# Kernel tuning notes

Hardware: AMD Instinct MI355X
Metric: run time of the kernel (lower is better)

## Reference

```python
import jax, jax.numpy as jnp
import numpy as np


def setup_inputs() -> dict:
    key = jax.random.key(0)
    k1, k2 = jax.random.split(key)
    B, C, H, W_, P = 32, 256, 64, 64, 8
    x = jax.random.normal(k1, (B, C, H, W_), dtype=jnp.float32)
    # 1x1 conv weight [P, C] and bias [P], init like torch Conv2d default
    bound = 1.0 / np.sqrt(C)
    W = jax.random.uniform(k2, (P, C), dtype=jnp.float32, minval=-bound, maxval=bound)
    b = jnp.zeros((P,), dtype=jnp.float32)
    return {"x": x, "W": W, "b": b}


def reference(x, W, b):
    B, C, H, Wd = x.shape
    P = W.shape[0]
    # 1x1 conv: scores[b,p,h,w] = sum_c W[p,c] * x[b,c,h,w] + b[p]
    scores = jnp.einsum('pc,bchw->bphw', W, x) + b[None, :, None, None]
    # spatial softmax over HW
    part_maps = jax.nn.softmax(scores.reshape(B, P, H * Wd), axis=2).reshape(B, P, H, Wd)
    # fused per-part weighted average pool: mean over HW of x * map
    pooled = jnp.einsum('bchw,bphw->bpc', x, part_maps) / (H * Wd)  # [B,P,C]
    return pooled.reshape(B, P * C)
```

## Files before the change

kernel.cpp:

```cpp
#include <hip/hip_runtime.h>

#define HW 4096
#define NC 256
#define NP 8
#define NB 32
#define CHW 64
#define NCH 64

#define FMA4(acc, v, s)                  \
  acc.x = fmaf((v).x, (s), acc.x);       \
  acc.y = fmaf((v).y, (s), acc.y);       \
  acc.z = fmaf((v).z, (s), acc.z);       \
  acc.w = fmaf((v).w, (s), acc.w)

__global__ __launch_bounds__(256) void k_fused(
    const float* __restrict__ x, const float* __restrict__ Wm,
    const float* __restrict__ bias, float* __restrict__ partial,
    float* __restrict__ psum) {
  __shared__ __align__(16) float wt[NC][NP];
  __shared__ __align__(16) float sp[4][NP][CHW];
  __shared__ __align__(16) float els[NP][68];

  const int bid = blockIdx.x;
  const int b = bid >> 6;
  const int chunk = bid & 63;
  const int t = threadIdx.x, lane = t & 63, w = t >> 6;
  const float* xb = x + (size_t)b * NC * HW + chunk * CHW;

#pragma unroll
  for (int p = 0; p < NP; ++p) wt[t][p] = Wm[p * NC + t];
  __syncthreads();

  const int cr = lane >> 4;
  const int q = lane & 15;
  const int c0 = w << 6;
  const float* xwp = xb + (size_t)(c0 + cr) * HW + q * 4;

  float4 s4[NP];
#pragma unroll
  for (int p = 0; p < NP; ++p) s4[p] = make_float4(0.f, 0.f, 0.f, 0.f);

#pragma unroll
  for (int h = 0; h < 2; ++h) {
    float4 xv[8];
#pragma unroll
    for (int i = 0; i < 8; ++i)
      xv[i] = *(const float4*)(xwp + (size_t)(h * 32 + i * 4) * HW);
#pragma unroll
    for (int i = 0; i < 8; ++i) {
      int c = c0 + h * 32 + i * 4 + cr;
      float4 wA = *(const float4*)&wt[c][0];
      float4 wB = *(const float4*)&wt[c][4];
      FMA4(s4[0], xv[i], wA.x);
      FMA4(s4[1], xv[i], wA.y);
      FMA4(s4[2], xv[i], wA.z);
      FMA4(s4[3], xv[i], wA.w);
      FMA4(s4[4], xv[i], wB.x);
      FMA4(s4[5], xv[i], wB.y);
      FMA4(s4[6], xv[i], wB.z);
      FMA4(s4[7], xv[i], wB.w);
    }
  }

#pragma unroll
  for (int p = 0; p < NP; ++p) {
    float4 v = s4[p];
    v.x += __shfl_xor(v.x, 16); v.y += __shfl_xor(v.y, 16);
    v.z += __shfl_xor(v.z, 16); v.w += __shfl_xor(v.w, 16);
    v.x += __shfl_xor(v.x, 32); v.y += __shfl_xor(v.y, 32);
    v.z += __shfl_xor(v.z, 32); v.w += __shfl_xor(v.w, 32);
    if (cr == 0) *(float4*)&sp[w][p][q * 4] = v;
  }
  __syncthreads();

  {
    const int ep = t >> 5, eh = t & 31;
    float a0 = bias[ep], a1 = a0;
#pragma unroll
    for (int ww = 0; ww < 4; ++ww) {
      a0 += sp[ww][ep][eh];
      a1 += sp[ww][ep][eh + 32];
    }
    float e0 = expf(a0), e1 = expf(a1);
    els[ep][eh] = e0;
    els[ep][eh + 32] = e1;
    float esum = e0 + e1;
#pragma unroll
    for (int off = 16; off; off >>= 1) esum += __shfl_xor(esum, off);
    if (eh == 0) psum[bid * NP + ep] = esum;
  }
  __syncthreads();

  const float* xr = xb + (size_t)t * HW;
  float acc[NP];
#pragma unroll
  for (int p = 0; p < NP; ++p) acc[p] = 0.f;

#pragma unroll
  for (int h = 0; h < 2; ++h) {
    float4 xv[8];
#pragma unroll
    for (int j = 0; j < 8; ++j)
      xv[j] = *(const float4*)(xr + (h * 8 + j) * 4);
#pragma unroll
    for (int j = 0; j < 8; ++j) {
      const int k = h * 8 + j;
#pragma unroll
      for (int p = 0; p < NP; ++p) {
        float4 e4 = *(const float4*)&els[p][k * 4];
        acc[p] = fmaf(xv[j].x, e4.x, acc[p]);
        acc[p] = fmaf(xv[j].y, e4.y, acc[p]);
        acc[p] = fmaf(xv[j].z, e4.z, acc[p]);
        acc[p] = fmaf(xv[j].w, e4.w, acc[p]);
      }
    }
  }

#pragma unroll
  for (int p = 0; p < NP; ++p)
    partial[((size_t)bid * NP + p) * NC + t] = acc[p];
}

__global__ __launch_bounds__(256) void k_reduce(
    const float* __restrict__ partial, const float* __restrict__ psum,
    float* __restrict__ out) {
  int bp = blockIdx.x;
  int b = bp >> 3, p = bp & 7;
  int t = threadIdx.x, lane = t & 63, w2 = t >> 6;

  __shared__ float gv;
  if (w2 == 0) {
    float v = psum[(size_t)(b * NCH + lane) * NP + p];
#pragma unroll
    for (int off = 32; off; off >>= 1) v += __shfl_xor(v, off);
    if (lane == 0) gv = 1.0f / (v * (float)HW);
  }
  __syncthreads();
  float ginv = gv;

  float acc = 0.f;
#pragma unroll 16
  for (int ch = 0; ch < NCH; ++ch)
    acc += partial[(((size_t)b * NCH + ch) * NP + p) * NC + t];
  out[((size_t)b * NP + p) * NC + t] = acc * ginv;
}

extern "C" void kernel_launch(void* const* d_in, const int* in_sizes, int n_in,
                              void* d_out, int out_size, void* d_ws, size_t ws_size,
                              hipStream_t stream) {
  const float* x = (const float*)d_in[0];
  const float* Wm = (const float*)d_in[1];
  const float* bias = (const float*)d_in[2];
  float* out = (float*)d_out;

  float* ws = (float*)d_ws;
  float* partial = ws;
  float* psum = ws + (size_t)NB * NCH * NP * NC;

  k_fused<<<NB * NCH, 256, 0, stream>>>(x, Wm, bias, partial, psum);
  k_reduce<<<NB * NP, 256, 0, stream>>>(partial, psum, out);
}
```

Measured before the change: 52.31 us.

## Process two 64-pixel subchunks per block, prefetching second subchunk during pooling

Each block now covers 128 spatial positions as two 64-wide subchunks, which halves the block count and the size of the partial buffer that the reduce kernel must sum. The first half of the second subchunk's x loads is issued before the first subchunk's pooling pass, so those global reads overlap with compute. It uses double-buffered exp tiles in shared memory and accumulates pooled sums across both subchunks. In exchange, the prefetched registers raise register pressure, and there are fewer blocks to fill the GPU.

```diff
diff --git a/kernel.cpp b/kernel.cpp
--- a/kernel.cpp
+++ b/kernel.cpp
@@ -4,8 +4,9 @@
 #define NC 256
 #define NP 8
 #define NB 32
-#define CHW 64
-#define NCH 64
+#define SUB 64
+#define CHW 128
+#define NCH (HW / CHW)
 
 #define FMA4(acc, v, s)                  \
   acc.x = fmaf((v).x, (s), acc.x);       \
@@ -13,17 +14,33 @@
   acc.z = fmaf((v).z, (s), acc.z);       \
   acc.w = fmaf((v).w, (s), acc.w)
 
+#define A_BATCH(xvarr, hbase)                                  \
+  _Pragma("unroll")                                            \
+  for (int i = 0; i < 8; ++i) {                                \
+    int c = c0 + (hbase) + i * 4 + cr;                         \
+    float4 wA = *(const float4*)&wt[c][0];                     \
+    float4 wB = *(const float4*)&wt[c][4];                     \
+    FMA4(s4[0], xvarr[i], wA.x);                               \
+    FMA4(s4[1], xvarr[i], wA.y);                               \
+    FMA4(s4[2], xvarr[i], wA.z);                               \
+    FMA4(s4[3], xvarr[i], wA.w);                               \
+    FMA4(s4[4], xvarr[i], wB.x);                               \
+    FMA4(s4[5], xvarr[i], wB.y);                               \
+    FMA4(s4[6], xvarr[i], wB.z);                               \
+    FMA4(s4[7], xvarr[i], wB.w);                               \
+  }
+
 __global__ __launch_bounds__(256) void k_fused(
     const float* __restrict__ x, const float* __restrict__ Wm,
     const float* __restrict__ bias, float* __restrict__ partial,
     float* __restrict__ psum) {
   __shared__ __align__(16) float wt[NC][NP];
-  __shared__ __align__(16) float sp[4][NP][CHW];
-  __shared__ __align__(16) float els[NP][68];
+  __shared__ __align__(16) float sp[4][NP][SUB];
+  __shared__ __align__(16) float els[2][NP][68];
 
   const int bid = blockIdx.x;
-  const int b = bid >> 6;
-  const int chunk = bid & 63;
+  const int b = bid >> 5;
+  const int chunk = bid & 31;
   const int t = threadIdx.x, lane = t & 63, w = t >> 6;
   const float* xb = x + (size_t)b * NC * HW + chunk * CHW;
 
@@ -34,34 +51,28 @@
   const int cr = lane >> 4;
   const int q = lane & 15;
   const int c0 = w << 6;
-  const float* xwp = xb + (size_t)(c0 + cr) * HW + q * 4;
+  const int ep = t >> 5, eh = t & 31;
+  const float bia = bias[ep];
+  const float* xwp0 = xb + (size_t)(c0 + cr) * HW + q * 4;
+  const float* xwp1 = xwp0 + SUB;
+  const float* xr = xb + (size_t)t * HW;
+
+  float acc[NP];
+#pragma unroll
+  for (int p = 0; p < NP; ++p) acc[p] = 0.f;
+  float esum_tot = 0.f;
 
   float4 s4[NP];
 #pragma unroll
   for (int p = 0; p < NP; ++p) s4[p] = make_float4(0.f, 0.f, 0.f, 0.f);
-
 #pragma unroll
   for (int h = 0; h < 2; ++h) {
     float4 xv[8];
 #pragma unroll
     for (int i = 0; i < 8; ++i)
-      xv[i] = *(const float4*)(xwp + (size_t)(h * 32 + i * 4) * HW);
-#pragma unroll
-    for (int i = 0; i < 8; ++i) {
-      int c = c0 + h * 32 + i * 4 + cr;
-      float4 wA = *(const float4*)&wt[c][0];
-      float4 wB = *(const float4*)&wt[c][4];
-      FMA4(s4[0], xv[i], wA.x);
-      FMA4(s4[1], xv[i], wA.y);
-      FMA4(s4[2], xv[i], wA.z);
-      FMA4(s4[3], xv[i], wA.w);
-      FMA4(s4[4], xv[i], wB.x);
-      FMA4(s4[5], xv[i], wB.y);
-      FMA4(s4[6], xv[i], wB.z);
-      FMA4(s4[7], xv[i], wB.w);
-    }
-  }
-
+      xv[i] = *(const float4*)(xwp0 + (size_t)(h * 32 + i * 4) * HW);
+    A_BATCH(xv, h * 32)
+  }
 #pragma unroll
   for (int p = 0; p < NP; ++p) {
     float4 v = s4[p];
@@ -74,27 +85,23 @@
   __syncthreads();
 
   {
-    const int ep = t >> 5, eh = t & 31;
-    float a0 = bias[ep], a1 = a0;
+    float a0 = bia, a1 = bia;
 #pragma unroll
     for (int ww = 0; ww < 4; ++ww) {
       a0 += sp[ww][ep][eh];
       a1 += sp[ww][ep][eh + 32];
     }
     float e0 = expf(a0), e1 = expf(a1);
-    els[ep][eh] = e0;
-    els[ep][eh + 32] = e1;
-    float esum = e0 + e1;
-#pragma unroll
-    for (int off = 16; off; off >>= 1) esum += __shfl_xor(esum, off);
-    if (eh == 0) psum[bid * NP + ep] = esum;
-  }
-  __syncthreads();
-
-  const float* xr = xb + (size_t)t * HW;
-  float acc[NP];
-#pragma unroll
-  for (int p = 0; p < NP; ++p) acc[p] = 0.f;
+    els[0][ep][eh] = e0;
+    els[0][ep][eh + 32] = e1;
+    esum_tot += e0 + e1;
+  }
+  __syncthreads();
+
+  float4 xp[8];
+#pragma unroll
+  for (int i = 0; i < 8; ++i)
+    xp[i] = *(const float4*)(xwp1 + (size_t)(i * 4) * HW);
 
 #pragma unroll
   for (int h = 0; h < 2; ++h) {
@@ -107,7 +114,7 @@
       const int k = h * 8 + j;
 #pragma unroll
       for (int p = 0; p < NP; ++p) {
-        float4 e4 = *(const float4*)&els[p][k * 4];
+        float4 e4 = *(const float4*)&els[0][p][k * 4];
         acc[p] = fmaf(xv[j].x, e4.x, acc[p]);
         acc[p] = fmaf(xv[j].y, e4.y, acc[p]);
         acc[p] = fmaf(xv[j].z, e4.z, acc[p]);
@@ -117,8 +124,67 @@
   }
 
 #pragma unroll
+  for (int p = 0; p < NP; ++p) s4[p] = make_float4(0.f, 0.f, 0.f, 0.f);
+  A_BATCH(xp, 0)
+  {
+    float4 xv[8];
+#pragma unroll
+    for (int i = 0; i < 8; ++i)
+      xv[i] = *(const float4*)(xwp1 + (size_t)(32 + i * 4) * HW);
+    A_BATCH(xv, 32)
+  }
+#pragma unroll
+  for (int p = 0; p < NP; ++p) {
+    float4 v = s4[p];
+    v.x += __shfl_xor(v.x, 16); v.y += __shfl_xor(v.y, 16);
+    v.z += __shfl_xor(v.z, 16); v.w += __shfl_xor(v.w, 16);
+    v.x += __shfl_xor(v.x, 32); v.y += __shfl_xor(v.y, 32);
+    v.z += __shfl_xor(v.z, 32); v.w += __shfl_xor(v.w, 32);
+    if (cr == 0) *(float4*)&sp[w][p][q * 4] = v;
+  }
+  __syncthreads();
+
+  {
+    float a0 = bia, a1 = bia;
+#pragma unroll
+    for (int ww = 0; ww < 4; ++ww) {
+      a0 += sp[ww][ep][eh];
+      a1 += sp[ww][ep][eh + 32];
+    }
+    float e0 = expf(a0), e1 = expf(a1);
+    els[1][ep][eh] = e0;
+    els[1][ep][eh + 32] = e1;
+    esum_tot += e0 + e1;
+  }
+  __syncthreads();
+
+#pragma unroll
+  for (int h = 0; h < 2; ++h) {
+    float4 xv[8];
+#pragma unroll
+    for (int j = 0; j < 8; ++j)
+      xv[j] = *(const float4*)(xr + SUB + (h * 8 + j) * 4);
+#pragma unroll
+    for (int j = 0; j < 8; ++j) {
+      const int k = h * 8 + j;
+#pragma unroll
+      for (int p = 0; p < NP; ++p) {
+        float4 e4 = *(const float4*)&els[1][p][k * 4];
+        acc[p] = fmaf(xv[j].x, e4.x, acc[p]);
+        acc[p] = fmaf(xv[j].y, e4.y, acc[p]);
+        acc[p] = fmaf(xv[j].z, e4.z, acc[p]);
+        acc[p] = fmaf(xv[j].w, e4.w, acc[p]);
+      }
+    }
+  }
+
+#pragma unroll
   for (int p = 0; p < NP; ++p)
     partial[((size_t)bid * NP + p) * NC + t] = acc[p];
+
+#pragma unroll
+  for (int off = 16; off; off >>= 1) esum_tot += __shfl_xor(esum_tot, off);
+  if (eh == 0) psum[bid * NP + ep] = esum_tot;
 }
 
 __global__ __launch_bounds__(256) void k_reduce(
@@ -130,9 +196,9 @@
 
   __shared__ float gv;
   if (w2 == 0) {
-    float v = psum[(size_t)(b * NCH + lane) * NP + p];
-#pragma unroll
-    for (int off = 32; off; off >>= 1) v += __shfl_xor(v, off);
+    float v = (lane < NCH) ? psum[(size_t)(b * NCH + lane) * NP + p] : 0.f;
+#pragma unroll
+    for (int off = 16; off; off >>= 1) v += __shfl_xor(v, off);
     if (lane == 0) gv = 1.0f / (v * (float)HW);
   }
   __syncthreads();
```

After: 193.2 us. 3.69x slower.

## Stage x tile in swizzled LDS to avoid re-reading global memory in pooling pass

Applied to the files above, without the earlier changes.

During the score pass, each block now writes its loaded x tile (256 channels by 64 positions) into shared memory, using an XOR swizzle to avoid bank conflicts. The pooling pass then reads x from LDS instead of fetching it from global memory a second time. The weight table and the exp table now share one buffer, because their lifetimes do not overlap. The cost is roughly 80KB of LDS per block, which sharply limits how many blocks can be resident per CU and may reduce latency hiding.

```diff
diff --git a/kernel.cpp b/kernel.cpp
--- a/kernel.cpp
+++ b/kernel.cpp
@@ -13,13 +13,32 @@
   acc.z = fmaf((v).z, (s), acc.z);       \
   acc.w = fmaf((v).w, (s), acc.w)
 
+#define WT(c, pp) wt_els[(c) * NP + (pp)]
+#define ELS(pp, hw) wt_els[(pp) * 64 + (hw)]
+
+#define A_BATCH(xvarr, hbase)                                  \
+  _Pragma("unroll")                                            \
+  for (int i = 0; i < 8; ++i) {                                \
+    int c = c0 + (hbase) + i * 4 + cr;                         \
+    float4 wA = *(const float4*)&WT(c, 0);                     \
+    float4 wB = *(const float4*)&WT(c, 4);                     \
+    FMA4(s4[0], xvarr[i], wA.x);                               \
+    FMA4(s4[1], xvarr[i], wA.y);                               \
+    FMA4(s4[2], xvarr[i], wA.z);                               \
+    FMA4(s4[3], xvarr[i], wA.w);                               \
+    FMA4(s4[4], xvarr[i], wB.x);                               \
+    FMA4(s4[5], xvarr[i], wB.y);                               \
+    FMA4(s4[6], xvarr[i], wB.z);                               \
+    FMA4(s4[7], xvarr[i], wB.w);                               \
+  }
+
 __global__ __launch_bounds__(256) void k_fused(
     const float* __restrict__ x, const float* __restrict__ Wm,
     const float* __restrict__ bias, float* __restrict__ partial,
     float* __restrict__ psum) {
-  __shared__ __align__(16) float wt[NC][NP];
+  __shared__ __align__(16) float xs[NC][64];
   __shared__ __align__(16) float sp[4][NP][CHW];
-  __shared__ __align__(16) float els[NP][68];
+  __shared__ __align__(16) float wt_els[NC * NP];
 
   const int bid = blockIdx.x;
   const int b = bid >> 6;
@@ -28,7 +47,7 @@
   const float* xb = x + (size_t)b * NC * HW + chunk * CHW;
 
 #pragma unroll
-  for (int p = 0; p < NP; ++p) wt[t][p] = Wm[p * NC + t];
+  for (int p = 0; p < NP; ++p) WT(t, p) = Wm[p * NC + t];
   __syncthreads();
 
   const int cr = lane >> 4;
@@ -49,17 +68,9 @@
 #pragma unroll
     for (int i = 0; i < 8; ++i) {
       int c = c0 + h * 32 + i * 4 + cr;
-      float4 wA = *(const float4*)&wt[c][0];
-      float4 wB = *(const float4*)&wt[c][4];
-      FMA4(s4[0], xv[i], wA.x);
-      FMA4(s4[1], xv[i], wA.y);
-      FMA4(s4[2], xv[i], wA.z);
-      FMA4(s4[3], xv[i], wA.w);
-      FMA4(s4[4], xv[i], wB.x);
-      FMA4(s4[5], xv[i], wB.y);
-      FMA4(s4[6], xv[i], wB.z);
-      FMA4(s4[7], xv[i], wB.w);
+      *(float4*)&xs[c][(q ^ (c & 7)) << 2] = xv[i];
     }
+    A_BATCH(xv, h * 32)
   }
 
 #pragma unroll
@@ -82,8 +93,8 @@
       a1 += sp[ww][ep][eh + 32];
     }
     float e0 = expf(a0), e1 = expf(a1);
-    els[ep][eh] = e0;
-    els[ep][eh + 32] = e1;
+    ELS(ep, eh) = e0;
+    ELS(ep, eh + 32) = e1;
     float esum = e0 + e1;
 #pragma unroll
     for (int off = 16; off; off >>= 1) esum += __shfl_xor(esum, off);
@@ -91,7 +102,7 @@
   }
   __syncthreads();
 
-  const float* xr = xb + (size_t)t * HW;
+  const int tk = t & 7;
   float acc[NP];
 #pragma unroll
   for (int p = 0; p < NP; ++p) acc[p] = 0.f;
@@ -100,14 +111,16 @@
   for (int h = 0; h < 2; ++h) {
     float4 xv[8];
 #pragma unroll
-    for (int j = 0; j < 8; ++j)
-      xv[j] = *(const float4*)(xr + (h * 8 + j) * 4);
+    for (int j = 0; j < 8; ++j) {
+      int k = h * 8 + j;
+      xv[j] = *(const float4*)&xs[t][(k ^ tk) << 2];
+    }
 #pragma unroll
     for (int j = 0; j < 8; ++j) {
       const int k = h * 8 + j;
 #pragma unroll
       for (int p = 0; p < NP; ++p) {
-        float4 e4 = *(const float4*)&els[p][k * 4];
+        float4 e4 = *(const float4*)&ELS(p, k * 4);
         acc[p] = fmaf(xv[j].x, e4.x, acc[p]);
         acc[p] = fmaf(xv[j].y, e4.y, acc[p]);
         acc[p] = fmaf(xv[j].z, e4.z, acc[p]);
```

New measurement: 48.22 us. -7.8%, faster.

## Keep x tile in registers for both conv and pooling passes, processing two sub-spans

Applied to the files above, without the earlier changes.

Each block now handles its 64-pixel span as two 32-pixel sub-spans. The x values loaded for the 1x1 conv scores stay in registers and are reused for the softmax-weighted pooling, so x is no longer read a second time. Per-thread accumulators grow to 8x8 and need a shuffle reduction before the partial results are written, which raises register pressure. Launch bounds now request 3 blocks per SM to balance occupancy against that pressure.

```diff
diff --git a/kernel.cpp b/kernel.cpp
--- a/kernel.cpp
+++ b/kernel.cpp
@@ -4,8 +4,10 @@
 #define NC 256
 #define NP 8
 #define NB 32
-#define CHW 64
-#define NCH 64
+#define SUBHW 32
+#define SPAN 64
+#define NSP 64
+#define NBLK (NB * NSP)
 
 #define FMA4(acc, v, s)                  \
   acc.x = fmaf((v).x, (s), acc.x);       \
@@ -13,44 +15,52 @@
   acc.z = fmaf((v).z, (s), acc.z);       \
   acc.w = fmaf((v).w, (s), acc.w)
 
-__global__ __launch_bounds__(256) void k_fused(
+__global__ __launch_bounds__(256, 3) void k_fused(
     const float* __restrict__ x, const float* __restrict__ Wm,
     const float* __restrict__ bias, float* __restrict__ partial,
     float* __restrict__ psum) {
   __shared__ __align__(16) float wt[NC][NP];
-  __shared__ __align__(16) float sp[4][NP][CHW];
-  __shared__ __align__(16) float els[NP][68];
+  __shared__ __align__(16) float sp[4][NP][SUBHW];
+  __shared__ __align__(16) float els[NP][SUBHW];
 
   const int bid = blockIdx.x;
   const int b = bid >> 6;
-  const int chunk = bid & 63;
+  const int span = bid & 63;
   const int t = threadIdx.x, lane = t & 63, w = t >> 6;
-  const float* xb = x + (size_t)b * NC * HW + chunk * CHW;
+  const int cr = lane >> 3;
+  const int q = lane & 7;
+  const int c0 = w << 6;
+  const int ep = t >> 5, eh = t & 31;
 
 #pragma unroll
   for (int p = 0; p < NP; ++p) wt[t][p] = Wm[p * NC + t];
+
+  const float* xq = x + (size_t)b * NC * HW + span * SPAN + q * 4;
+  const float bia = bias[ep];
+
+  float acc[8][NP];
+#pragma unroll
+  for (int i = 0; i < 8; ++i)
+#pragma unroll
+    for (int p = 0; p < NP; ++p) acc[i][p] = 0.f;
+  float esum_tot = 0.f;
+
   __syncthreads();
 
-  const int cr = lane >> 4;
-  const int q = lane & 15;
-  const int c0 = w << 6;
-  const float* xwp = xb + (size_t)(c0 + cr) * HW + q * 4;
-
-  float4 s4[NP];
-#pragma unroll
-  for (int p = 0; p < NP; ++p) s4[p] = make_float4(0.f, 0.f, 0.f, 0.f);
-
-#pragma unroll
-  for (int h = 0; h < 2; ++h) {
+#pragma unroll 1
+  for (int k = 0; k < 2; ++k) {
     float4 xv[8];
 #pragma unroll
     for (int i = 0; i < 8; ++i)
-      xv[i] = *(const float4*)(xwp + (size_t)(h * 32 + i * 4) * HW);
+      xv[i] = *(const float4*)(xq + k * SUBHW + (size_t)(c0 + 8 * i + cr) * HW);
+
+    float4 s4[NP];
+#pragma unroll
+    for (int p = 0; p < NP; ++p) s4[p] = make_float4(0.f, 0.f, 0.f, 0.f);
 #pragma unroll
     for (int i = 0; i < 8; ++i) {
-      int c = c0 + h * 32 + i * 4 + cr;
-      float4 wA = *(const float4*)&wt[c][0];
-      float4 wB = *(const float4*)&wt[c][4];
+      const float4 wA = *(const float4*)&wt[c0 + 8 * i + cr][0];
+      const float4 wB = *(const float4*)&wt[c0 + 8 * i + cr][4];
       FMA4(s4[0], xv[i], wA.x);
       FMA4(s4[1], xv[i], wA.y);
       FMA4(s4[2], xv[i], wA.z);
@@ -60,65 +70,66 @@
       FMA4(s4[6], xv[i], wB.z);
       FMA4(s4[7], xv[i], wB.w);
     }
-  }
 
 #pragma unroll
-  for (int p = 0; p < NP; ++p) {
-    float4 v = s4[p];
-    v.x += __shfl_xor(v.x, 16); v.y += __shfl_xor(v.y, 16);
-    v.z += __shfl_xor(v.z, 16); v.w += __shfl_xor(v.w, 16);
-    v.x += __shfl_xor(v.x, 32); v.y += __shfl_xor(v.y, 32);
-    v.z += __shfl_xor(v.z, 32); v.w += __shfl_xor(v.w, 32);
-    if (cr == 0) *(float4*)&sp[w][p][q * 4] = v;
-  }
-  __syncthreads();
+    for (int p = 0; p < NP; ++p) {
+      float4 v = s4[p];
+      v.x += __shfl_xor(v.x, 8);  v.y += __shfl_xor(v.y, 8);
+      v.z += __shfl_xor(v.z, 8);  v.w += __shfl_xor(v.w, 8);
+      v.x += __shfl_xor(v.x, 16); v.y += __shfl_xor(v.y, 16);
+      v.z += __shfl_xor(v.z, 16); v.w += __shfl_xor(v.w, 16);
+      v.x += __shfl_xor(v.x, 32); v.y += __shfl_xor(v.y, 32);
+      v.z += __shfl_xor(v.z, 32); v.w += __shfl_xor(v.w, 32);
+      if (cr == 0) *(float4*)&sp[w][p][q * 4] = v;
+    }
+    __syncthreads();
 
-  {
-    const int ep = t >> 5, eh = t & 31;
-    float a0 = bias[ep], a1 = a0;
+    {
+      float a = bia;
 #pragma unroll
-    for (int ww = 0; ww < 4; ++ww) {
-      a0 += sp[ww][ep][eh];
-      a1 += sp[ww][ep][eh + 32];
+      for (int ww = 0; ww < 4; ++ww) a += sp[ww][ep][eh];
+      float e0 = expf(a);
+      els[ep][eh] = e0;
+      esum_tot += e0;
     }
-    float e0 = expf(a0), e1 = expf(a1);
-    els[ep][eh] = e0;
-    els[ep][eh + 32] = e1;
-    float esum = e0 + e1;
-#pragma unroll
-    for (int off = 16; off; off >>= 1) esum += __shfl_xor(esum, off);
-    if (eh == 0) psum[bid * NP + ep] = esum;
-  }
-  __syncthreads();
-
-  const float* xr = xb + (size_t)t * HW;
-  float acc[NP];
-#pragma unroll
-  for (int p = 0; p < NP; ++p) acc[p] = 0.f;
+    __syncthreads();
 
 #pragma unroll
-  for (int h = 0; h < 2; ++h) {
-    float4 xv[8];
+    for (int p = 0; p < NP; ++p) {
+      const float4 e4 = *(const float4*)&els[p][q * 4];
 #pragma unroll
-    for (int j = 0; j < 8; ++j)
-      xv[j] = *(const float4*)(xr + (h * 8 + j) * 4);
-#pragma unroll
-    for (int j = 0; j < 8; ++j) {
-      const int k = h * 8 + j;
-#pragma unroll
-      for (int p = 0; p < NP; ++p) {
-        float4 e4 = *(const float4*)&els[p][k * 4];
-        acc[p] = fmaf(xv[j].x, e4.x, acc[p]);
-        acc[p] = fmaf(xv[j].y, e4.y, acc[p]);
-        acc[p] = fmaf(xv[j].z, e4.z, acc[p]);
-        acc[p] = fmaf(xv[j].w, e4.w, acc[p]);
+      for (int i = 0; i < 8; ++i) {
+        acc[i][p] = fmaf(xv[i].x, e4.x, acc[i][p]);
+        acc[i][p] = fmaf(xv[i].y, e4.y, acc[i][p]);
+        acc[i][p] = fmaf(xv[i].z, e4.z, acc[i][p]);
+        acc[i][p] = fmaf(xv[i].w, e4.w, acc[i][p]);
       }
     }
   }
 
 #pragma unroll
-  for (int p = 0; p < NP; ++p)
-    partial[((size_t)bid * NP + p) * NC + t] = acc[p];
+  for (int i = 0; i < 8; ++i)
+#pragma unroll
+    for (int p = 0; p < NP; ++p) {
+      float v = acc[i][p];
+      v += __shfl_xor(v, 1);
+      v += __shfl_xor(v, 2);
+      v += __shfl_xor(v, 4);
+      acc[i][p] = v;
+    }
+  if (q == 0) {
+#pragma unroll
+    for (int i = 0; i < 8; ++i) {
+      const int c = c0 + 8 * i + cr;
+#pragma unroll
+      for (int p = 0; p < NP; ++p)
+        partial[((size_t)bid * NP + p) * NC + c] = acc[i][p];
+    }
+  }
+
+#pragma unroll
+  for (int off = 16; off; off >>= 1) esum_tot += __shfl_xor(esum_tot, off);
+  if (eh == 0) psum[bid * NP + ep] = esum_tot;
 }
 
 __global__ __launch_bounds__(256) void k_reduce(
@@ -130,7 +141,7 @@
 
   __shared__ float gv;
   if (w2 == 0) {
-    float v = psum[(size_t)(b * NCH + lane) * NP + p];
+    float v = psum[(size_t)(b * NSP + lane) * NP + p];
 #pragma unroll
     for (int off = 32; off; off >>= 1) v += __shfl_xor(v, off);
     if (lane == 0) gv = 1.0f / (v * (float)HW);
@@ -140,8 +151,8 @@
 
   float acc = 0.f;
 #pragma unroll 16
-  for (int ch = 0; ch < NCH; ++ch)
-    acc += partial[(((size_t)b * NCH + ch) * NP + p) * NC + t];
+  for (int ch = 0; ch < NSP; ++ch)
+    acc += partial[(((size_t)b * NSP + ch) * NP + p) * NC + t];
   out[((size_t)b * NP + p) * NC + t] = acc * ginv;
 }
 
@@ -155,8 +166,8 @@
 
   float* ws = (float*)d_ws;
   float* partial = ws;
-  float* psum = ws + (size_t)NB * NCH * NP * NC;
+  float* psum = ws + (size_t)NBLK * NP * NC;
 
-  k_fused<<<NB * NCH, 256, 0, stream>>>(x, Wm, bias, partial, psum);
+  k_fused<<<NBLK, 256, 0, stream>>>(x, Wm, bias, partial, psum);
   k_reduce<<<NB * NP, 256, 0, stream>>>(partial, psum, out);
 }
```

New measurement: 71.64 us. 37.0% more time.
